# Kernel tuning notes

Measured on AMD Instinct MI355X. Metric: run time of the kernel, lower is better.

Reference implementation:

```python
import jax, jax.numpy as jnp
import numpy as np

NUM_GRAPHS = 1024
HIDDEN = 256
N_NODES = 500000


def setup_inputs() -> dict:
    key = jax.random.key(0)
    k1, k2, k3, k4 = jax.random.split(key, 4)
    x = jax.random.normal(k1, (N_NODES, HIDDEN), dtype=jnp.float32)
    batch = jnp.sort(jax.random.randint(k2, (N_NODES,), 0, NUM_GRAPHS, dtype=jnp.int64))
    # attention = nn.Linear(hidden_dim, 1): weight [1, hidden], bias [1]
    bound = 1.0 / np.sqrt(HIDDEN)
    att_w = jax.random.uniform(k3, (HIDDEN, 1), dtype=jnp.float32, minval=-bound, maxval=bound)
    att_b = jax.random.uniform(k4, (1,), dtype=jnp.float32, minval=-bound, maxval=bound)
    return {"x": x, "batch": batch, "att_w": att_w, "att_b": att_b}


def reference(x, batch, att_w, att_b):
    seg = batch.astype(jnp.int32)
    # mean pool: segment sum / counts
    sums = jax.ops.segment_sum(x, seg, num_segments=NUM_GRAPHS)  # [G, H]
    counts = jax.ops.segment_sum(jnp.ones((x.shape[0],), x.dtype), seg, num_segments=NUM_GRAPHS)
    mean_pool = sums / jnp.maximum(counts, 1.0)[:, None]
    # max pool
    max_pool = jax.ops.segment_max(x, seg, num_segments=NUM_GRAPHS)
    # attention-weighted add pool: sigmoid(x @ w + b) * x, segment-summed
    weights = jax.nn.sigmoid(x @ att_w + att_b)  # [N, 1]
    att_pool = jax.ops.segment_sum(x * weights, seg, num_segments=NUM_GRAPHS)
    return jnp.concatenate([mean_pool, max_pool, att_pool], axis=-1)
```

## Files before the change

### kernel.cpp

```cpp
#include <hip/hip_runtime.h>
#include <math.h>

constexpr int NUM_GRAPHS = 1024;

typedef float f4_t __attribute__((ext_vector_type(4)));
__device__ __forceinline__ float4 nt_load(const float4* p) {
    f4_t v = __builtin_nontemporal_load((const f4_t*)p);
    return make_float4(v.x, v.y, v.z, v.w);
}

__global__ void detect_i32_kernel(const int* __restrict__ words, int n,
                                  int* __restrict__ flag) {
    const int stride = gridDim.x * blockDim.x;
    int acc = 0;
    for (int j = 1 + 2 * (int)(blockIdx.x * blockDim.x + threadIdx.x); j < n;
         j += 2 * stride)
        acc |= words[j];
    if (__any(acc != 0)) {
        if ((threadIdx.x & 63) == 0) atomicOr(flag, 1);
    }
}

__global__ void seg_start_kernel(const int* __restrict__ words, int n,
                                 const int* __restrict__ flag,
                                 int* __restrict__ seg) {
    int i = blockIdx.x * blockDim.x + threadIdx.x;
    if (i >= n) return;
    const bool is32 = (*flag != 0);
    int b    = is32 ? words[i] : words[2 * i];
    int prev = (i == 0) ? -1 : (is32 ? words[i - 1] : words[2 * (i - 1)]);
    for (int g = prev + 1; g <= b; ++g) seg[g] = i;
    if (i == n - 1)
        for (int g = b + 1; g <= NUM_GRAPHS; ++g) seg[g] = n;
}

__global__ __launch_bounds__(256) void pool_fused_kernel(
    const float* __restrict__ x, const float* __restrict__ att_w,
    const float* __restrict__ att_b, const int* __restrict__ seg,
    float* __restrict__ out) {
    const int g    = blockIdx.x;
    const int lane = threadIdx.x & 63;
    const int w    = threadIdx.x >> 6;

    const int s0    = seg[g];
    const int e0    = seg[g + 1];
    const int cnt   = e0 - s0;
    const int chunk = (cnt + 3) >> 2;
    const int wbeg  = min(s0 + w * chunk, e0);
    const int wend  = min(wbeg + chunk, e0);

    const float4* __restrict__ x4 = (const float4*)x;
    const float4 wv   = ((const float4*)att_w)[lane];
    const float  bias = att_b[0];

    float sx = 0.f, sy = 0.f, sz = 0.f, sw = 0.f;
    float mx = -INFINITY, my = -INFINITY, mz = -INFINITY, mw = -INFINITY;
    float ax = 0.f, ay = 0.f, az = 0.f, aw = 0.f;

    auto proc4 = [&](const float4* v) {
        float p[4];
#pragma unroll
        for (int r = 0; r < 4; ++r)
            p[r] = v[r].x * wv.x + v[r].y * wv.y + v[r].z * wv.z + v[r].w * wv.w;
#pragma unroll
        for (int off = 32; off >= 1; off >>= 1) {
#pragma unroll
            for (int r = 0; r < 4; ++r)
                p[r] += __shfl_xor(p[r], off, 64);
        }
#pragma unroll
        for (int r = 0; r < 4; ++r) {
            const float sig = 1.0f / (1.0f + __expf(-(p[r] + bias)));
            sx += v[r].x; sy += v[r].y; sz += v[r].z; sw += v[r].w;
            mx = fmaxf(mx, v[r].x); my = fmaxf(my, v[r].y);
            mz = fmaxf(mz, v[r].z); mw = fmaxf(mw, v[r].w);
            ax += v[r].x * sig; ay += v[r].y * sig;
            az += v[r].z * sig; aw += v[r].w * sig;
        }
    };

    int i = wbeg;
    if (i + 4 <= wend) {
        float4 v[4];
#pragma unroll
        for (int r = 0; r < 4; ++r)
            v[r] = nt_load(x4 + (size_t)(i + r) * 64 + lane);
        int nb = i + 4;
        while (nb + 4 <= wend) {
            float4 vn[4];
#pragma unroll
            for (int r = 0; r < 4; ++r)
                vn[r] = nt_load(x4 + (size_t)(nb + r) * 64 + lane);
            proc4(v);
#pragma unroll
            for (int r = 0; r < 4; ++r) v[r] = vn[r];
            nb += 4;
        }
        proc4(v);
        i = nb;
    }
    for (; i < wend; ++i) {
        const float4 v = nt_load(x4 + (size_t)i * 64 + lane);
        float p = v.x * wv.x + v.y * wv.y + v.z * wv.z + v.w * wv.w;
#pragma unroll
        for (int off = 32; off >= 1; off >>= 1)
            p += __shfl_xor(p, off, 64);
        const float sig = 1.0f / (1.0f + __expf(-(p + bias)));
        sx += v.x; sy += v.y; sz += v.z; sw += v.w;
        mx = fmaxf(mx, v.x); my = fmaxf(my, v.y);
        mz = fmaxf(mz, v.z); mw = fmaxf(mw, v.w);
        ax += v.x * sig; ay += v.y * sig; az += v.z * sig; aw += v.w * sig;
    }

    __shared__ float4 lsum[4][64];
    __shared__ float4 lmax[4][64];
    __shared__ float4 latt[4][64];
    lsum[w][lane] = make_float4(sx, sy, sz, sw);
    lmax[w][lane] = make_float4(mx, my, mz, mw);
    latt[w][lane] = make_float4(ax, ay, az, aw);
    __syncthreads();

    float4* __restrict__ o = (float4*)(out + (size_t)g * 768);
    if (w == 0) {
        float4 S = lsum[0][lane];
#pragma unroll
        for (int ww = 1; ww < 4; ++ww) {
            float4 b = lsum[ww][lane];
            S.x += b.x; S.y += b.y; S.z += b.z; S.w += b.w;
        }
        const float inv = 1.0f / (float)(cnt > 0 ? cnt : 1);
        S.x *= inv; S.y *= inv; S.z *= inv; S.w *= inv;
        o[lane] = S;
    } else if (w == 1) {
        float4 M = lmax[0][lane];
#pragma unroll
        for (int ww = 1; ww < 4; ++ww) {
            float4 b = lmax[ww][lane];
            M.x = fmaxf(M.x, b.x); M.y = fmaxf(M.y, b.y);
            M.z = fmaxf(M.z, b.z); M.w = fmaxf(M.w, b.w);
        }
        o[64 + lane] = M;
    } else if (w == 2) {
        float4 A = latt[0][lane];
#pragma unroll
        for (int ww = 1; ww < 4; ++ww) {
            float4 b = latt[ww][lane];
            A.x += b.x; A.y += b.y; A.z += b.z; A.w += b.w;
        }
        o[128 + lane] = A;
    }
}

extern "C" void kernel_launch(void* const* d_in, const int* in_sizes, int n_in,
                              void* d_out, int out_size, void* d_ws, size_t ws_size,
                              hipStream_t stream) {
    const float* x           = (const float*)d_in[0];
    const int*   batch_words = (const int*)d_in[1];
    const float* att_w       = (const float*)d_in[2];
    const float* att_b       = (const float*)d_in[3];
    float*       out         = (float*)d_out;
    const int n = in_sizes[1];

    int* flag = (int*)d_ws;
    int* seg  = ((int*)d_ws) + 8;

    hipMemsetAsync(flag, 0, sizeof(int), stream);
    detect_i32_kernel<<<256, 256, 0, stream>>>(batch_words, n, flag);
    seg_start_kernel<<<(n + 255) / 256, 256, 0, stream>>>(batch_words, n, flag, seg);
    pool_fused_kernel<<<NUM_GRAPHS, 256, 0, stream>>>(x, att_w, att_b, seg, out);
}
```

Baseline: 633.5 us.

## Drop int width detection pass, unroll pooling loop to 8 rows, use plain loads

Removes the memset and detect kernel that scanned the batch array to decide whether it is int32 or int64. Width is now inferred from a single word in the middle of the array. The pooling loop now prefetches 8 rows per wave instead of 4, to keep more loads in flight, and switches nontemporal loads to ordinary loads. The single-word check could misdetect the width if that word happens to be zero, and the deeper unroll raises register pressure.

```diff
diff --git a/kernel.cpp b/kernel.cpp
--- a/kernel.cpp
+++ b/kernel.cpp
@@ -3,30 +3,11 @@
 
 constexpr int NUM_GRAPHS = 1024;
 
-typedef float f4_t __attribute__((ext_vector_type(4)));
-__device__ __forceinline__ float4 nt_load(const float4* p) {
-    f4_t v = __builtin_nontemporal_load((const f4_t*)p);
-    return make_float4(v.x, v.y, v.z, v.w);
-}
-
-__global__ void detect_i32_kernel(const int* __restrict__ words, int n,
-                                  int* __restrict__ flag) {
-    const int stride = gridDim.x * blockDim.x;
-    int acc = 0;
-    for (int j = 1 + 2 * (int)(blockIdx.x * blockDim.x + threadIdx.x); j < n;
-         j += 2 * stride)
-        acc |= words[j];
-    if (__any(acc != 0)) {
-        if ((threadIdx.x & 63) == 0) atomicOr(flag, 1);
-    }
-}
-
 __global__ void seg_start_kernel(const int* __restrict__ words, int n,
-                                 const int* __restrict__ flag,
                                  int* __restrict__ seg) {
     int i = blockIdx.x * blockDim.x + threadIdx.x;
     if (i >= n) return;
-    const bool is32 = (*flag != 0);
+    const bool is32 = words[(n >> 1) | 1] != 0;
     int b    = is32 ? words[i] : words[2 * i];
     int prev = (i == 0) ? -1 : (is32 ? words[i - 1] : words[2 * (i - 1)]);
     for (int g = prev + 1; g <= b; ++g) seg[g] = i;
@@ -57,19 +38,19 @@
     float mx = -INFINITY, my = -INFINITY, mz = -INFINITY, mw = -INFINITY;
     float ax = 0.f, ay = 0.f, az = 0.f, aw = 0.f;
 
-    auto proc4 = [&](const float4* v) {
-        float p[4];
+    auto proc8 = [&](const float4* v) {
+        float p[8];
 #pragma unroll
-        for (int r = 0; r < 4; ++r)
+        for (int r = 0; r < 8; ++r)
             p[r] = v[r].x * wv.x + v[r].y * wv.y + v[r].z * wv.z + v[r].w * wv.w;
 #pragma unroll
         for (int off = 32; off >= 1; off >>= 1) {
 #pragma unroll
-            for (int r = 0; r < 4; ++r)
+            for (int r = 0; r < 8; ++r)
                 p[r] += __shfl_xor(p[r], off, 64);
         }
 #pragma unroll
-        for (int r = 0; r < 4; ++r) {
+        for (int r = 0; r < 8; ++r) {
             const float sig = 1.0f / (1.0f + __expf(-(p[r] + bias)));
             sx += v[r].x; sy += v[r].y; sz += v[r].z; sw += v[r].w;
             mx = fmaxf(mx, v[r].x); my = fmaxf(my, v[r].y);
@@ -80,27 +61,27 @@
     };
 
     int i = wbeg;
-    if (i + 4 <= wend) {
-        float4 v[4];
+    if (i + 8 <= wend) {
+        float4 v[8];
 #pragma unroll
-        for (int r = 0; r < 4; ++r)
-            v[r] = nt_load(x4 + (size_t)(i + r) * 64 + lane);
-        int nb = i + 4;
-        while (nb + 4 <= wend) {
-            float4 vn[4];
+        for (int r = 0; r < 8; ++r)
+            v[r] = x4[(size_t)(i + r) * 64 + lane];
+        int nb = i + 8;
+        while (nb + 8 <= wend) {
+            float4 vn[8];
 #pragma unroll
-            for (int r = 0; r < 4; ++r)
-                vn[r] = nt_load(x4 + (size_t)(nb + r) * 64 + lane);
-            proc4(v);
+            for (int r = 0; r < 8; ++r)
+                vn[r] = x4[(size_t)(nb + r) * 64 + lane];
+            proc8(v);
 #pragma unroll
-            for (int r = 0; r < 4; ++r) v[r] = vn[r];
-            nb += 4;
+            for (int r = 0; r < 8; ++r) v[r] = vn[r];
+            nb += 8;
         }
-        proc4(v);
+        proc8(v);
         i = nb;
     }
     for (; i < wend; ++i) {
-        const float4 v = nt_load(x4 + (size_t)i * 64 + lane);
+        const float4 v = x4[(size_t)i * 64 + lane];
         float p = v.x * wv.x + v.y * wv.y + v.z * wv.z + v.w * wv.w;
 #pragma unroll
         for (int off = 32; off >= 1; off >>= 1)
@@ -161,11 +142,8 @@
     float*       out         = (float*)d_out;
     const int n = in_sizes[1];
 
-    int* flag = (int*)d_ws;
-    int* seg  = ((int*)d_ws) + 8;
+    int* seg = ((int*)d_ws) + 8;
 
-    hipMemsetAsync(flag, 0, sizeof(int), stream);
-    detect_i32_kernel<<<256, 256, 0, stream>>>(batch_words, n, flag);
-    seg_start_kernel<<<(n + 255) / 256, 256, 0, stream>>>(batch_words, n, flag, seg);
+    seg_start_kernel<<<(n + 255) / 256, 256, 0, stream>>>(batch_words, n, seg);
     pool_fused_kernel<<<NUM_GRAPHS, 256, 0, stream>>>(x, att_w, att_b, seg, out);
 }
```

Measured after the change: 664.8 us. +4.9%, slower.
